# Optimization experiments

Measured on AMD Instinct MI355X. Metric: run time of the kernel, lower is better.

Reference implementation:

```python
import jax, jax.numpy as jnp
import numpy as np

LEAKY = 0.01   # torch LeakyReLU default negative_slope
BN_EPS = 1e-5  # torch BatchNorm1d default eps


def _batchnorm(x, gamma, beta):
    # train-mode BatchNorm1d: normalize with per-batch biased statistics
    mean = jnp.mean(x, axis=0)
    var = jnp.var(x, axis=0)
    return (x - mean) * jax.lax.rsqrt(var + BN_EPS) * gamma + beta


def setup_inputs() -> dict:
    key = jax.random.key(0)
    ks = jax.random.split(key, 8)
    B, F, depth = 32768, 1, 10
    n_nodes = 2 ** depth  # 1024
    x = jax.random.normal(ks[0], (B, F), jnp.float32)
    prenet_w1 = jax.random.normal(ks[1], (16, F), jnp.float32) * 0.5
    prenet_b1 = jax.random.normal(ks[2], (16,), jnp.float32) * 0.1
    bn1_gamma = jnp.ones((16,), jnp.float32)
    bn1_beta = jnp.zeros((16,), jnp.float32)
    prenet_w2 = jax.random.normal(ks[3], (F, 16), jnp.float32) * 0.25
    prenet_b2 = jax.random.normal(ks[4], (F,), jnp.float32) * 0.1
    bn2_gamma = jnp.ones((F,), jnp.float32)
    bn2_beta = jnp.zeros((F,), jnp.float32)
    fc_w = jax.random.normal(ks[5], (n_nodes, F, F), jnp.float32) * 0.5
    fc_b = jax.random.normal(ks[6], (n_nodes, F), jnp.float32) * 0.1
    return {
        'x': x,
        'prenet_w1': prenet_w1, 'prenet_b1': prenet_b1,
        'bn1_gamma': bn1_gamma, 'bn1_beta': bn1_beta,
        'prenet_w2': prenet_w2, 'prenet_b2': prenet_b2,
        'bn2_gamma': bn2_gamma, 'bn2_beta': bn2_beta,
        'fc_w': fc_w, 'fc_b': fc_b,
    }


def reference(x, prenet_w1, prenet_b1, bn1_gamma, bn1_beta,
              prenet_w2, prenet_b2, bn2_gamma, bn2_beta, fc_w, fc_b):
    # prenet: Linear -> LeakyReLU -> BN -> Linear -> LeakyReLU -> BN
    h = jax.nn.leaky_relu(x @ prenet_w1.T + prenet_b1, LEAKY)
    h = _batchnorm(h, bn1_gamma, bn1_beta)
    h = jax.nn.leaky_relu(h @ prenet_w2.T + prenet_b2, LEAKY)
    x = _batchnorm(h, bn2_gamma, bn2_beta)

    # per-node Linear + sigmoid, fused as one batched GEMM:
    # (B,F) x (n_nodes,F,F) -> (B, n_nodes, F); here F == 1
    d = jax.nn.sigmoid(jnp.einsum('bf,nof->bno', x, fc_w) + fc_b)
    decision = jnp.concatenate([d, 1.0 - d], axis=2)  # (B, n_nodes, 2)

    B = x.shape[0]
    depth = int(np.log2(fc_w.shape[0]))
    mu = jnp.ones((B, 2, 1), x.dtype)
    begin, end = 1, 2
    for n_layer in range(depth):  # small fixed loop over tree depth
        # route parent probs to both children: (B, 2^n, 2)
        nu = jnp.tile(mu[:, begin:, :], (1, 1, 2)) * decision[:, begin:end, :]
        begin, end = end, end + 2 ** (n_layer + 1)
        mu = jnp.concatenate([mu, nu.reshape(B, -1, 1)], axis=1)
    mu = mu[..., 0]           # (B, 2^(depth+1))
    return mu.at[:, 0].set(0.0)
```

## Files before the change

### kernel.cpp

```cpp
#include <hip/hip_runtime.h>

#define LEAKY_S 0.01f
#define BN_EPS 1e-5f
#define LOG2E 1.44269504088896340736f

typedef float f32x2 __attribute__((ext_vector_type(2)));
typedef float f32x4 __attribute__((ext_vector_type(4)));

__device__ __forceinline__ float leaky(float v) { return v >= 0.0f ? v : LEAKY_S * v; }
__device__ __forceinline__ float fast_exp2(float v) { return __builtin_amdgcn_exp2f(v); }
__device__ __forceinline__ float sig2(float z2) {
    return __builtin_amdgcn_rcpf(1.0f + fast_exp2(-z2));
}
__device__ __forceinline__ void st4(float* p, float a, float b, float c, float d) {
    f32x4 v = {a, b, c, d}; *(f32x4*)p = v;
}

__global__ __launch_bounds__(256) void k_part1(const float* __restrict__ x,
        const float* __restrict__ w1, const float* __restrict__ b1,
        float* __restrict__ p1, int B) {
    float w1r[16], b1r[16], s[16], q[16];
#pragma unroll
    for (int j = 0; j < 16; ++j) { w1r[j] = w1[j]; b1r[j] = b1[j]; s[j] = 0.f; q[j] = 0.f; }
    int tid = threadIdx.x;
    int i = blockIdx.x * 256 + tid;
    if (2 * i < B) {
        f32x2 xv = *(const f32x2*)(x + 2 * i);
#pragma unroll
        for (int e = 0; e < 2; ++e) {
#pragma unroll
            for (int j = 0; j < 16; ++j) {
                float h = leaky(fmaf(xv[e], w1r[j], b1r[j]));
                s[j] += h; q[j] += h * h;
            }
        }
    }
#pragma unroll
    for (int j = 0; j < 16; ++j) {
        for (int off = 32; off >= 1; off >>= 1) {
            s[j] += __shfl_xor(s[j], off, 64);
            q[j] += __shfl_xor(q[j], off, 64);
        }
    }
    __shared__ float red[4][32];
    int w = tid >> 6, lane = tid & 63;
    if (lane == 0) {
#pragma unroll
        for (int j = 0; j < 16; ++j) { red[w][j] = s[j]; red[w][j + 16] = q[j]; }
    }
    __syncthreads();
    if (tid < 32)
        p1[blockIdx.x * 32 + tid] = red[0][tid] + red[1][tid] + red[2][tid] + red[3][tid];
}

__device__ __forceinline__ void fold_bn1(const float* __restrict__ p1,
        const float* __restrict__ w2, const float* __restrict__ b2,
        const float* __restrict__ g1, const float* __restrict__ be1,
        float* coef, int tid, float invB) {
    float acc = 0.f;
    for (int i = 0; i < 64; ++i) acc += p1[i * 32 + tid];
    float qacc = __shfl(acc, tid + 16, 64);
    float cp = 0.f;
    if (tid < 16) {
        float mean = acc * invB;
        float var  = qacc * invB - mean * mean;
        float inv  = rsqrtf(var + BN_EPS) * g1[tid];
        float sh   = fmaf(-mean, inv, be1[tid]);
        coef[tid] = inv * w2[tid];
        cp = sh * w2[tid];
    }
    for (int off = 8; off >= 1; off >>= 1) cp += __shfl_xor(cp, off, 16);
    if (tid == 0) coef[16] = cp + b2[0];
}

__global__ __launch_bounds__(256) void k_h2f(const float* __restrict__ x,
        const float* __restrict__ w1, const float* __restrict__ b1,
        const float* __restrict__ p1, const float* __restrict__ w2,
        const float* __restrict__ b2, const float* __restrict__ g1,
        const float* __restrict__ be1, float* __restrict__ p2,
        float* __restrict__ cfws, int B, float invB) {
    __shared__ float coef[17];
    int tid = threadIdx.x;
    if (tid < 32) fold_bn1(p1, w2, b2, g1, be1, coef, tid, invB);
    __syncthreads();
    if (blockIdx.x == 0 && tid < 17) cfws[tid] = coef[tid];
    float w1r[16], b1r[16], ar[16];
#pragma unroll
    for (int j = 0; j < 16; ++j) { w1r[j] = w1[j]; b1r[j] = b1[j]; ar[j] = coef[j]; }
    float c0 = coef[16];
    float s = 0.f, q = 0.f;
    int i = blockIdx.x * 256 + tid;
    if (2 * i < B) {
        f32x2 xv = *(const f32x2*)(x + 2 * i);
#pragma unroll
        for (int e = 0; e < 2; ++e) {
            float acc = c0;
#pragma unroll
            for (int j = 0; j < 16; ++j) {
                float h = leaky(fmaf(xv[e], w1r[j], b1r[j]));
                acc = fmaf(h, ar[j], acc);
            }
            float h2 = leaky(acc);
            s += h2; q += h2 * h2;
        }
    }
    for (int off = 32; off >= 1; off >>= 1) {
        s += __shfl_xor(s, off, 64);
        q += __shfl_xor(q, off, 64);
    }
    __shared__ float red[4][2];
    int w = tid >> 6, lane = tid & 63;
    if (lane == 0) { red[w][0] = s; red[w][1] = q; }
    __syncthreads();
    if (tid == 0) {
        p2[blockIdx.x * 2 + 0] = red[0][0] + red[1][0] + red[2][0] + red[3][0];
        p2[blockIdx.x * 2 + 1] = red[0][1] + red[1][1] + red[2][1] + red[3][1];
    }
}

__global__ __launch_bounds__(256, 4) void k_tree(const float* __restrict__ x,
        const float* __restrict__ w1, const float* __restrict__ b1,
        const float* __restrict__ g2, const float* __restrict__ be2,
        const float* __restrict__ fcw, const float* __restrict__ fcb,
        const float* __restrict__ p2, const float* __restrict__ cfws,
        float* __restrict__ out, int B, float invB) {
    __shared__ float wl[1024], bl[1024];
    __shared__ float x2s[16];
    __shared__ float bn2[2];
    int tid = threadIdx.x;

    for (int i = tid; i < 1024; i += 256) {
        int d;
        if (i < 128)      d = i;
        else if (i < 256) { int o = i - 128; d = 128 + ((o & 1) << 6) + (o >> 1); }
        else if (i < 512) { int o = i - 256; d = 256 + ((((o >> 7) << 1) | (o & 1)) << 6) + ((o & 127) >> 1); }
        else              { int o = i - 512; d = 512 + ((((o >> 7) << 1) | (o & 1)) << 6) + ((o & 127) >> 1); }
        wl[d] = fcw[i];
        bl[d] = fcb[i];
    }
    if (tid < 64) {
        float s = p2[2 * tid], q = p2[2 * tid + 1];
        for (int off = 32; off >= 1; off >>= 1) {
            s += __shfl_xor(s, off, 64);
            q += __shfl_xor(q, off, 64);
        }
        if (tid == 0) {
            float mean = s * invB, var = q * invB - mean * mean;
            float inv = rsqrtf(var + BN_EPS) * g2[0];
            bn2[0] = inv;
            bn2[1] = fmaf(-mean, inv, be2[0]);
        }
    }
    if (tid >= 64 && tid < 80) {
        int rr = tid - 64;
        int r = blockIdx.x * 16 + rr;
        float xv = (r < B) ? x[r] : 0.f;
        float acc = cfws[16];
#pragma unroll
        for (int j = 0; j < 16; ++j) {
            float h = leaky(fmaf(xv, w1[j], b1[j]));
            acc = fmaf(h, cfws[j], acc);
        }
        x2s[rr] = leaky(acc);
    }
    __syncthreads();
    {
        float s2k = bn2[0] * LOG2E, t2 = bn2[1];
        for (int i = tid; i < 1024; i += 256) {
            float wv = wl[i];
            wl[i] = wv * s2k;
            bl[i] = fmaf(t2, wv, bl[i]) * LOG2E;
        }
    }
    __syncthreads();

    const int w = tid >> 6, lane = tid & 63;
#pragma unroll 1
    for (int it = 0; it < 4; ++it) {
        const int r = blockIdx.x * 16 + w * 4 + it;
        const bool act = r < B;
        const float x2 = x2s[w * 4 + it];
        float* op = out + (size_t)r * 2048;

        float s0q[4];
        float mup;
        {
            float z = fmaf(x2, wl[1], bl[1]);
            float pz = sig2(z);
            float c0 = pz, c1 = 1.0f - pz;
            if (lane == 0) { s0q[0] = 0.f; s0q[1] = 1.f; s0q[2] = c0; s0q[3] = c1; }
            mup = (lane & 1) ? c1 : c0;
        }
#pragma unroll
        for (int l = 2; l <= 6; ++l) {
            const int P = 1 << (l - 1);
            float wv = wl[P + lane], bv = bl[P + lane];
            float z = fmaf(x2, wv, bv);
            float pz = sig2(z);
            float c0 = mup * pz, c1 = mup - c0;
            int sk = (2 * lane - P) & 63;
            float g0 = __shfl(c0, sk, 64);
            float g1 = __shfl(c1, sk, 64);
            float g2 = __shfl(c0, sk + 1, 64);
            float g3 = __shfl(c1, sk + 1, 64);
            if (lane >= P / 2 && lane < P) { s0q[0] = g0; s0q[1] = g1; s0q[2] = g2; s0q[3] = g3; }
            float n0 = __shfl(c0, lane >> 1, 64);
            float n1 = __shfl(c1, lane >> 1, 64);
            mup = (lane & 1) ? n1 : n0;
        }
        float c2v[2];
        {
            float wv = wl[64 + lane], bv = bl[64 + lane];
            float z = fmaf(x2, wv, bv);
            float pz = sig2(z);
            c2v[0] = mup * pz;
            c2v[1] = mup - c2v[0];
            int sk = (2 * lane - 64) & 63;
            float g0 = __shfl(c2v[0], sk, 64);
            float g1 = __shfl(c2v[1], sk, 64);
            float g2 = __shfl(c2v[0], sk + 1, 64);
            float g3 = __shfl(c2v[1], sk + 1, 64);
            if (lane >= 32) { s0q[0] = g0; s0q[1] = g1; s0q[2] = g2; s0q[3] = g3; }
        }
        float c4v[4];
#pragma unroll
        for (int s = 0; s < 2; ++s) {
            float wv = wl[128 + (s << 6) + lane], bv = bl[128 + (s << 6) + lane];
            float z = fmaf(x2, wv, bv);
            float pz = sig2(z);
            c4v[2 * s]     = c2v[s] * pz;
            c4v[2 * s + 1] = c2v[s] - c4v[2 * s];
        }
        float c8v[2][4];
#pragma unroll
        for (int j2 = 0; j2 < 2; ++j2) {
            int src = (j2 << 5) + (lane >> 1);
            float A  = __shfl(c4v[0], src, 64);
            float Bv = __shfl(c4v[1], src, 64);
            float C  = __shfl(c4v[2], src, 64);
            float D  = __shfl(c4v[3], src, 64);
            float m0 = (lane & 1) ? C : A;
            float m1 = (lane & 1) ? D : Bv;
            float wv0 = wl[256 + ((2 * j2) << 6) + lane],     bv0 = bl[256 + ((2 * j2) << 6) + lane];
            float wv1 = wl[256 + ((2 * j2 + 1) << 6) + lane], bv1 = bl[256 + ((2 * j2 + 1) << 6) + lane];
            float z0 = fmaf(x2, wv0, bv0);
            float z1 = fmaf(x2, wv1, bv1);
            float p0 = sig2(z0), p1v = sig2(z1);
            c8v[j2][0] = m0 * p0;
            c8v[j2][1] = m0 - c8v[j2][0];
            c8v[j2][2] = m1 * p1v;
            c8v[j2][3] = m1 - c8v[j2][2];
        }
        float l10[4][4];
#pragma unroll
        for (int j = 0; j < 4; ++j) {
            const int j2 = j >> 1;
            int src = ((j & 1) << 5) + (lane >> 1);
            float A  = __shfl(c8v[j2][0], src, 64);
            float Bv = __shfl(c8v[j2][1], src, 64);
            float C  = __shfl(c8v[j2][2], src, 64);
            float D  = __shfl(c8v[j2][3], src, 64);
            float m0 = (lane & 1) ? C : A;
            float m1 = (lane & 1) ? D : Bv;
            float wv0 = wl[512 + ((2 * j) << 6) + lane],     bv0 = bl[512 + ((2 * j) << 6) + lane];
            float wv1 = wl[512 + ((2 * j + 1) << 6) + lane], bv1 = bl[512 + ((2 * j + 1) << 6) + lane];
            float z0 = fmaf(x2, wv0, bv0);
            float z1 = fmaf(x2, wv1, bv1);
            float p0 = sig2(z0), p1v = sig2(z1);
            l10[j][0] = m0 * p0;
            l10[j][1] = m0 - l10[j][0];
            l10[j][2] = m1 * p1v;
            l10[j][3] = m1 - l10[j][2];
        }
        if (act) {
            const int o4 = lane << 2;
            st4(op + o4,        s0q[0],    s0q[1],    s0q[2],    s0q[3]);
            st4(op + 256 + o4,  c4v[0],    c4v[1],    c4v[2],    c4v[3]);
            st4(op + 512 + o4,  c8v[0][0], c8v[0][1], c8v[0][2], c8v[0][3]);
            st4(op + 768 + o4,  c8v[1][0], c8v[1][1], c8v[1][2], c8v[1][3]);
            st4(op + 1024 + o4, l10[0][0], l10[0][1], l10[0][2], l10[0][3]);
            st4(op + 1280 + o4, l10[1][0], l10[1][1], l10[1][2], l10[1][3]);
            st4(op + 1536 + o4, l10[2][0], l10[2][1], l10[2][2], l10[2][3]);
            st4(op + 1792 + o4, l10[3][0], l10[3][1], l10[3][2], l10[3][3]);
        }
    }
}

extern "C" void kernel_launch(void* const* d_in, const int* in_sizes, int n_in,
                              void* d_out, int out_size, void* d_ws, size_t ws_size,
                              hipStream_t stream) {
    const float* x   = (const float*)d_in[0];
    const float* w1  = (const float*)d_in[1];
    const float* b1  = (const float*)d_in[2];
    const float* g1  = (const float*)d_in[3];
    const float* be1 = (const float*)d_in[4];
    const float* w2  = (const float*)d_in[5];
    const float* b2  = (const float*)d_in[6];
    const float* g2  = (const float*)d_in[7];
    const float* be2 = (const float*)d_in[8];
    const float* fcw = (const float*)d_in[9];
    const float* fcb = (const float*)d_in[10];
    float* out = (float*)d_out;
    int B = in_sizes[0];
    float invB = 1.0f / (float)B;

    float* ws = (float*)d_ws;
    float* p1 = ws;
    float* p2 = ws + 2048;
    float* cf = ws + 2176;

    k_part1<<<64, 256, 0, stream>>>(x, w1, b1, p1, B);
    k_h2f  <<<64, 256, 0, stream>>>(x, w1, b1, p1, w2, b2, g1, be1, p2, cf, B, invB);

    int blocks = (B + 15) / 16;
    k_tree<<<blocks, 256, 0, stream>>>(x, w1, b1, g2, be2, fcw, fcb, p2, cf,
                                       out, B, invB);
}
```

Before: 57.31 us.

## Merge BN statistics kernels via cooperative grid sync and double rows per tree block

Fuses the two BatchNorm-statistics kernels into one cooperative kernel that uses a grid-wide sync between the first-layer moments and the second-layer moments. This removes one kernel launch and reuses the loaded x and w1/b1 registers. The tree kernel now handles 32 rows per block instead of 16, halving the block count so the per-block shared-memory weight staging and BN folding are amortised over more rows. In exchange the cooperative launch and grid barrier add their own overhead, and fewer blocks means less parallelism in the tree stage.

```diff
diff --git a/kernel.cpp b/kernel.cpp
--- a/kernel.cpp
+++ b/kernel.cpp
@@ -1,4 +1,5 @@
 #include <hip/hip_runtime.h>
+#include <hip/hip_cooperative_groups.h>
 
 #define LEAKY_S 0.01f
 #define BN_EPS 1e-5f
@@ -14,43 +15,6 @@
 }
 __device__ __forceinline__ void st4(float* p, float a, float b, float c, float d) {
     f32x4 v = {a, b, c, d}; *(f32x4*)p = v;
-}
-
-__global__ __launch_bounds__(256) void k_part1(const float* __restrict__ x,
-        const float* __restrict__ w1, const float* __restrict__ b1,
-        float* __restrict__ p1, int B) {
-    float w1r[16], b1r[16], s[16], q[16];
-#pragma unroll
-    for (int j = 0; j < 16; ++j) { w1r[j] = w1[j]; b1r[j] = b1[j]; s[j] = 0.f; q[j] = 0.f; }
-    int tid = threadIdx.x;
-    int i = blockIdx.x * 256 + tid;
-    if (2 * i < B) {
-        f32x2 xv = *(const f32x2*)(x + 2 * i);
-#pragma unroll
-        for (int e = 0; e < 2; ++e) {
-#pragma unroll
-            for (int j = 0; j < 16; ++j) {
-                float h = leaky(fmaf(xv[e], w1r[j], b1r[j]));
-                s[j] += h; q[j] += h * h;
-            }
-        }
-    }
-#pragma unroll
-    for (int j = 0; j < 16; ++j) {
-        for (int off = 32; off >= 1; off >>= 1) {
-            s[j] += __shfl_xor(s[j], off, 64);
-            q[j] += __shfl_xor(q[j], off, 64);
-        }
-    }
-    __shared__ float red[4][32];
-    int w = tid >> 6, lane = tid & 63;
-    if (lane == 0) {
-#pragma unroll
-        for (int j = 0; j < 16; ++j) { red[w][j] = s[j]; red[w][j + 16] = q[j]; }
-    }
-    __syncthreads();
-    if (tid < 32)
-        p1[blockIdx.x * 32 + tid] = red[0][tid] + red[1][tid] + red[2][tid] + red[3][tid];
 }
 
 __device__ __forceinline__ void fold_bn1(const float* __restrict__ p1,
@@ -73,25 +37,65 @@
     if (tid == 0) coef[16] = cp + b2[0];
 }
 
-__global__ __launch_bounds__(256) void k_h2f(const float* __restrict__ x,
+__global__ __launch_bounds__(256) void k_stats(const float* __restrict__ x,
         const float* __restrict__ w1, const float* __restrict__ b1,
-        const float* __restrict__ p1, const float* __restrict__ w2,
-        const float* __restrict__ b2, const float* __restrict__ g1,
-        const float* __restrict__ be1, float* __restrict__ p2,
+        const float* __restrict__ w2, const float* __restrict__ b2,
+        const float* __restrict__ g1, const float* __restrict__ be1,
+        float* __restrict__ p1, float* __restrict__ p2,
         float* __restrict__ cfws, int B, float invB) {
+    int tid = threadIdx.x;
+    float w1r[16], b1r[16];
+#pragma unroll
+    for (int j = 0; j < 16; ++j) { w1r[j] = w1[j]; b1r[j] = b1[j]; }
+    int i = blockIdx.x * 256 + tid;
+    f32x2 xv = {0.f, 0.f};
+    bool have = (2 * i < B);
+    if (have) xv = *(const f32x2*)(x + 2 * i);
+
+    {
+        float s[16], q[16];
+#pragma unroll
+        for (int j = 0; j < 16; ++j) { s[j] = 0.f; q[j] = 0.f; }
+        if (have) {
+#pragma unroll
+            for (int e = 0; e < 2; ++e) {
+#pragma unroll
+                for (int j = 0; j < 16; ++j) {
+                    float h = leaky(fmaf(xv[e], w1r[j], b1r[j]));
+                    s[j] += h; q[j] += h * h;
+                }
+            }
+        }
+#pragma unroll
+        for (int j = 0; j < 16; ++j) {
+            for (int off = 32; off >= 1; off >>= 1) {
+                s[j] += __shfl_xor(s[j], off, 64);
+                q[j] += __shfl_xor(q[j], off, 64);
+            }
+        }
+        __shared__ float red[4][32];
+        int w = tid >> 6, lane = tid & 63;
+        if (lane == 0) {
+#pragma unroll
+            for (int j = 0; j < 16; ++j) { red[w][j] = s[j]; red[w][j + 16] = q[j]; }
+        }
+        __syncthreads();
+        if (tid < 32)
+            p1[blockIdx.x * 32 + tid] = red[0][tid] + red[1][tid] + red[2][tid] + red[3][tid];
+    }
+
+    cooperative_groups::this_grid().sync();
+
     __shared__ float coef[17];
-    int tid = threadIdx.x;
     if (tid < 32) fold_bn1(p1, w2, b2, g1, be1, coef, tid, invB);
     __syncthreads();
     if (blockIdx.x == 0 && tid < 17) cfws[tid] = coef[tid];
-    float w1r[16], b1r[16], ar[16];
-#pragma unroll
-    for (int j = 0; j < 16; ++j) { w1r[j] = w1[j]; b1r[j] = b1[j]; ar[j] = coef[j]; }
+    float ar[16];
+#pragma unroll
+    for (int j = 0; j < 16; ++j) ar[j] = coef[j];
     float c0 = coef[16];
     float s = 0.f, q = 0.f;
-    int i = blockIdx.x * 256 + tid;
-    if (2 * i < B) {
-        f32x2 xv = *(const f32x2*)(x + 2 * i);
+    if (have) {
 #pragma unroll
         for (int e = 0; e < 2; ++e) {
             float acc = c0;
@@ -108,13 +112,13 @@
         s += __shfl_xor(s, off, 64);
         q += __shfl_xor(q, off, 64);
     }
-    __shared__ float red[4][2];
+    __shared__ float red2[4][2];
     int w = tid >> 6, lane = tid & 63;
-    if (lane == 0) { red[w][0] = s; red[w][1] = q; }
+    if (lane == 0) { red2[w][0] = s; red2[w][1] = q; }
     __syncthreads();
     if (tid == 0) {
-        p2[blockIdx.x * 2 + 0] = red[0][0] + red[1][0] + red[2][0] + red[3][0];
-        p2[blockIdx.x * 2 + 1] = red[0][1] + red[1][1] + red[2][1] + red[3][1];
+        p2[blockIdx.x * 2 + 0] = red2[0][0] + red2[1][0] + red2[2][0] + red2[3][0];
+        p2[blockIdx.x * 2 + 1] = red2[0][1] + red2[1][1] + red2[2][1] + red2[3][1];
     }
 }
 
@@ -125,7 +129,7 @@
         const float* __restrict__ p2, const float* __restrict__ cfws,
         float* __restrict__ out, int B, float invB) {
     __shared__ float wl[1024], bl[1024];
-    __shared__ float x2s[16];
+    __shared__ float x2s[32];
     __shared__ float bn2[2];
     int tid = threadIdx.x;
 
@@ -151,9 +155,9 @@
             bn2[1] = fmaf(-mean, inv, be2[0]);
         }
     }
-    if (tid >= 64 && tid < 80) {
+    if (tid >= 64 && tid < 96) {
         int rr = tid - 64;
-        int r = blockIdx.x * 16 + rr;
+        int r = blockIdx.x * 32 + rr;
         float xv = (r < B) ? x[r] : 0.f;
         float acc = cfws[16];
 #pragma unroll
@@ -176,10 +180,10 @@
 
     const int w = tid >> 6, lane = tid & 63;
 #pragma unroll 1
-    for (int it = 0; it < 4; ++it) {
-        const int r = blockIdx.x * 16 + w * 4 + it;
+    for (int it = 0; it < 8; ++it) {
+        const int r = blockIdx.x * 32 + w * 8 + it;
         const bool act = r < B;
-        const float x2 = x2s[w * 4 + it];
+        const float x2 = x2s[w * 8 + it];
         float* op = out + (size_t)r * 2048;
 
         float s0q[4];
@@ -309,10 +313,15 @@
     float* p2 = ws + 2048;
     float* cf = ws + 2176;
 
-    k_part1<<<64, 256, 0, stream>>>(x, w1, b1, p1, B);
-    k_h2f  <<<64, 256, 0, stream>>>(x, w1, b1, p1, w2, b2, g1, be1, p2, cf, B, invB);
-
-    int blocks = (B + 15) / 16;
+    void* args[] = {
+        (void*)&x, (void*)&w1, (void*)&b1, (void*)&w2, (void*)&b2,
+        (void*)&g1, (void*)&be1, (void*)&p1, (void*)&p2, (void*)&cf,
+        (void*)&B, (void*)&invB,
+    };
+    hipLaunchCooperativeKernel((void*)k_stats, dim3(64), dim3(256),
+                               args, 0, stream);
+
+    int blocks = (B + 31) / 32;
     k_tree<<<blocks, 256, 0, stream>>>(x, w1, b1, g2, be2, fcw, fcb, p2, cf,
                                        out, B, invB);
 }
```

Measured after the change: 85.00 us. +48.3%, slower.
